# Kernel tuning notes

Hardware: AMD Instinct MI355X
Metric: run time of the kernel (lower is better)

Reference implementation:

```python
import jax, jax.numpy as jnp
import numpy as np

TOP_K = 2
EPS = 1e-9


def setup_inputs() -> dict:
    key = jax.random.key(0)
    k1, k2, k3, k4 = jax.random.split(key, 4)
    B, T, D, H, E = 4, 2048, 1024, 4096, 8
    x = jax.random.normal(k1, (B, T, D), dtype=jnp.float32)
    Wr = jax.random.normal(k2, (D, E), dtype=jnp.float32) * 0.02
    W1 = jax.random.normal(k3, (E, D, H), dtype=jnp.float32) * 0.02
    W2 = jax.random.normal(k4, (E, H, D), dtype=jnp.float32) * 0.02
    return {"x": x, "Wr": Wr, "W1": W1, "W2": W2}


def reference(x, Wr, W1, W2):
    # x: (B,T,D); Wr: (D,E); W1: (E,D,H); W2: (E,H,D)
    E = Wr.shape[1]
    logits = jnp.einsum('btd,de->bte', x, Wr)          # (B,T,E)
    probs = jax.nn.softmax(logits, axis=-1)
    top_p, top_i = jax.lax.top_k(probs, TOP_K)         # (B,T,K)
    gates = top_p / (jnp.sum(top_p, axis=-1, keepdims=True) + EPS)
    # combine weights per expert: (B,T,E), zero where expert not selected
    oh = jax.nn.one_hot(top_i, E, dtype=x.dtype)       # (B,T,K,E)
    comb = jnp.sum(oh * gates[..., None], axis=2)      # (B,T,E)
    out = jnp.zeros_like(x)
    for e in range(E):  # fixed small expert loop
        h = jax.nn.gelu(jnp.einsum('btd,dh->bth', x, W1[e]), approximate=False)
        y = jnp.einsum('bth,hd->btd', h, W2[e])
        out = out + comb[..., e:e + 1] * y
    # load-balancing loss (on detached stats, matching torch .detach())
    mask = (jnp.sum(oh, axis=2) > 0).astype(jnp.float32)  # (B,T,E)
    imp = jnp.sum(jax.lax.stop_gradient(probs), axis=(0, 1))
    load = jnp.sum(jax.lax.stop_gradient(mask), axis=(0, 1))
    imp = imp / (jnp.sum(imp) + EPS)
    load = load / (jnp.sum(load) + EPS)
    lb = jnp.sum(imp * load) * E
    return out, lb
```

## Files before the change

### kernel.cpp

```cpp
#include <hip/hip_runtime.h>
#include <hip/hip_bf16.h>
#include <math.h>

#define NTOK 8192
#define DDIM 1024
#define HDIM 4096
#define NEXP 8
#define HROWS (NTOK*2 + 256)
#define RBLK 512

typedef unsigned int u32;
typedef unsigned short u16;
typedef __bf16 bf16x8 __attribute__((ext_vector_type(8)));
typedef float f32x4 __attribute__((ext_vector_type(4)));
typedef u16 u16x8 __attribute__((ext_vector_type(8)));
typedef u16 u16x4 __attribute__((ext_vector_type(4)));

__device__ __forceinline__ u16 f2bf(float f){
  u32 u = __builtin_bit_cast(u32, f);
  u32 r = (u + 0x7FFFu + ((u >> 16) & 1u)) >> 16;
  return (u16)r;
}
__device__ __forceinline__ float bf2f(u16 b){
  u32 u = ((u32)b) << 16;
  return __builtin_bit_cast(float, u);
}
__device__ __forceinline__ void gl_lds16(const void* g, void* l){
  __builtin_amdgcn_global_load_lds(
      (const __attribute__((address_space(1))) u32*)g,
      (__attribute__((address_space(3))) u32*)l, 16, 0, 0);
}
__device__ __forceinline__ float gelu_t(float v){
  float u = v * (0.7978845608f + 0.0356774081f * v * v);
  float e = __expf(2.0f * u);
  float t = 1.0f - 2.0f / (e + 1.0f);
  return 0.5f * v * (1.0f + t);
}

__global__ __launch_bounds__(256) void transpose_cvt(const float* __restrict__ in,
                                                     u16* __restrict__ out,
                                                     int R, int C){
  int e = blockIdx.z;
  const float* pin = in + (long)e * R * C;
  u16* pout = out + (long)e * R * C;
  __shared__ u16 tile[64][65];
  int c0 = blockIdx.x * 64, r0 = blockIdx.y * 64;
  int tid = threadIdx.x;
#pragma unroll
  for (int j = 0; j < 4; j++){
    int idx = tid + 256 * j;
    int r = idx >> 4, c4 = (idx & 15) << 2;
    float4 v = *(const float4*)(pin + (long)(r0 + r) * C + c0 + c4);
    tile[r][c4]     = f2bf(v.x);
    tile[r][c4 + 1] = f2bf(v.y);
    tile[r][c4 + 2] = f2bf(v.z);
    tile[r][c4 + 3] = f2bf(v.w);
  }
  __syncthreads();
#pragma unroll
  for (int j = 0; j < 4; j++){
    int idx = tid + 256 * j;
    int orow = idx >> 4, c4 = (idx & 15) << 2;
    u16x4 o;
    o[0] = tile[c4][orow];     o[1] = tile[c4 + 1][orow];
    o[2] = tile[c4 + 2][orow]; o[3] = tile[c4 + 3][orow];
    *(u16x4*)(pout + (long)(c0 + orow) * R + r0 + c4) = o;
  }
}

__global__ __launch_bounds__(1024) void route_kernel(const float* __restrict__ x,
                                                     const float* __restrict__ Wr,
                                                     u16* __restrict__ xb,
                                                     int4* __restrict__ meta,
                                                     float2* __restrict__ gates,
                                                     int* __restrict__ selrk,
                                                     int* __restrict__ blockhist,
                                                     float* __restrict__ impPart){
  const int wid = threadIdx.x >> 6;
  const int lane = threadIdx.x & 63;
  const int t = blockIdx.x * 16 + wid;
  const float* xr = x + (long)t * DDIM;
  u16* xbr = xb + (long)t * DDIM;
  float acc[NEXP] = {};
  for (int d0 = lane * 4; d0 < DDIM; d0 += 256){
    float4 xv = *(const float4*)(xr + d0);
    u16x4 xo;
    xo[0] = f2bf(xv.x); xo[1] = f2bf(xv.y); xo[2] = f2bf(xv.z); xo[3] = f2bf(xv.w);
    *(u16x4*)(xbr + d0) = xo;
    const float* w = Wr + d0 * NEXP;
#pragma unroll
    for (int q = 0; q < 4; q++){
      float xq = ((const float*)&xv)[q];
      float4 w0 = *(const float4*)(w + q * NEXP);
      float4 w1 = *(const float4*)(w + q * NEXP + 4);
      acc[0] += xq * w0.x; acc[1] += xq * w0.y; acc[2] += xq * w0.z; acc[3] += xq * w0.w;
      acc[4] += xq * w1.x; acc[5] += xq * w1.y; acc[6] += xq * w1.z; acc[7] += xq * w1.w;
    }
  }
#pragma unroll
  for (int e = 0; e < NEXP; e++){
#pragma unroll
    for (int off = 32; off; off >>= 1) acc[e] += __shfl_xor(acc[e], off, 64);
  }
  __shared__ int sel_s[32];
  __shared__ float p_s[16][NEXP];
  if (lane == 0){
    float mx = acc[0];
#pragma unroll
    for (int e = 1; e < NEXP; e++) mx = fmaxf(mx, acc[e]);
    float p[NEXP]; float s = 0.f;
#pragma unroll
    for (int e = 0; e < NEXP; e++){ p[e] = expf(acc[e] - mx); s += p[e]; }
    float inv = 1.f / s;
#pragma unroll
    for (int e = 0; e < NEXP; e++){ p[e] *= inv; p_s[wid][e] = p[e]; }
    int i0 = 0; float v0 = p[0];
#pragma unroll
    for (int e = 1; e < NEXP; e++) if (p[e] > v0){ v0 = p[e]; i0 = e; }
    int i1 = -1; float v1 = -1.f;
#pragma unroll
    for (int e = 0; e < NEXP; e++) if (e != i0 && p[e] > v1){ v1 = p[e]; i1 = e; }
    float gs = v0 + v1 + 1e-9f;
    meta[t] = make_int4(i0, i1, 0, 0);
    gates[t] = make_float2(v0 / gs, v1 / gs);
    sel_s[wid * 2] = i0;
    sel_s[wid * 2 + 1] = i1;
  }
  __syncthreads();
  const int tid = threadIdx.x;
  if (tid < 32){
    int e = sel_s[tid];
    int r = 0;
    for (int m = 0; m < tid; m++) r += (sel_s[m] == e) ? 1 : 0;
    selrk[blockIdx.x * 32 + tid] = (r << 3) | e;
  }
  if (tid < NEXP){
    int hcount = 0;
#pragma unroll
    for (int m = 0; m < 32; m++) hcount += (sel_s[m] == tid) ? 1 : 0;
    blockhist[blockIdx.x * NEXP + tid] = hcount;
    float s = 0.f;
#pragma unroll
    for (int w = 0; w < 16; w++) s += p_s[w][tid];
    impPart[blockIdx.x * NEXP + tid] = s;
  }
}

__global__ __launch_bounds__(512) void scan_kernel(int* __restrict__ blockhist,
                                                   const float* __restrict__ impPart,
                                                   int* __restrict__ cnt,
                                                   int* __restrict__ offs,
                                                   float* __restrict__ imp){
  const int e = threadIdx.x >> 6;
  const int lane = threadIdx.x & 63;
  const int base = lane * 8;
  int v[8]; int s = 0;
#pragma unroll
  for (int i = 0; i < 8; i++){
    int tmp = blockhist[(base + i) * NEXP + e];
    v[i] = s; s += tmp;
  }
  int inc = s;
#pragma unroll
  for (int off = 1; off < 64; off <<= 1){
    int o = __shfl_up(inc, off, 64);
    if (lane >= off) inc += o;
  }
  int excl = inc - s;
#pragma unroll
  for (int i = 0; i < 8; i++) blockhist[(base + i) * NEXP + e] = v[i] + excl;
  int tot = __shfl(inc, 63, 64);
  float fs = 0.f;
#pragma unroll
  for (int i = 0; i < 8; i++) fs += impPart[(base + i) * NEXP + e];
#pragma unroll
  for (int off = 32; off; off >>= 1) fs += __shfl_xor(fs, off, 64);
  __shared__ int cnt_s[NEXP];
  if (lane == 0){ cnt_s[e] = tot; cnt[e] = tot; imp[e] = fs; }
  __syncthreads();
  if (threadIdx.x == 0){
    int o = 0;
    for (int q = 0; q < NEXP; q++){ offs[q] = o; o += cnt_s[q]; }
  }
}

__global__ __launch_bounds__(256) void fill_kernel(const int* __restrict__ selrk,
                                                   const int* __restrict__ blockhist,
                                                   int* __restrict__ elist,
                                                   int4* __restrict__ meta){
  int m = blockIdx.x * 256 + threadIdx.x;
  int t = m >> 1, c = m & 1, b = m >> 5;
  int pk = selrk[m];
  int e = pk & 7, r = pk >> 3;
  int gslot = blockhist[b * NEXP + e] + r;
  elist[e * NTOK + gslot] = t;
  ((int*)meta)[t * 4 + 2 + c] = gslot;
}

template<int KD, int ND, bool GATHER, bool GELU>
__global__ __launch_bounds__(256) void gemm128_kernel(const u16* __restrict__ Ag,
                                                      const u16* __restrict__ Bg,
                                                      u16* __restrict__ Cg,
                                                      const int* __restrict__ elist,
                                                      const int* __restrict__ cnt,
                                                      const int* __restrict__ offs){
  const int NDB = ND / 128;
  const int bid = blockIdx.x;
  const int e  = bid & 7;
  const int le = bid >> 3;
  const int db = le % NDB;
  const int tt = le / NDB;
  const int n_e = cnt[e];
  if (tt * 128 >= n_e) return;
  const int cb = db * 128;
  __shared__ __align__(16) u16 As[128 * 64];
  __shared__ __align__(16) u16 Bs[128 * 64];
  const int tid = threadIdx.x;
  const int csrc = (((tid & 7) ^ ((tid >> 3) & 7)) << 3);
  const int clin = (tid & 7) << 3;
  const int row0 = offs[e] + tt * 128;
  const long bbase = ((long)e * ND + cb) * KD;
  long agb[4], bgb[4]; int lrow[4];
#pragma unroll
  for (int q = 0; q < 4; q++){
    int row = q * 32 + (tid >> 3);
    int arow;
    if (GATHER){
      int slot = tt * 128 + row;
      if (slot >= n_e) slot = n_e - 1;
      arow = elist[e * NTOK + slot];
    } else {
      arow = row0 + row;
    }
    lrow[q] = row;
    agb[q] = (long)arow * KD + csrc;
    bgb[q] = bbase + (long)row * KD + csrc;
  }
  const int wid = tid >> 6, lane = tid & 63;
  const int wr = (wid >> 1) * 64, wc = (wid & 1) * 64;
  const int fr = lane & 15, fq = lane >> 4;
  const int sw0 = (fq ^ (fr & 7)) << 3;
  const int sw1 = ((4 + fq) ^ (fr & 7)) << 3;
  const u16* aP0 = &As[(wr + fr) * 64 + sw0];
  const u16* aP1 = &As[(wr + fr) * 64 + sw1];
  const u16* bP0 = &Bs[(wc + fr) * 64 + sw0];
  const u16* bP1 = &Bs[(wc + fr) * 64 + sw1];
  f32x4 acc[4][4] = {};
  for (int kb = 0; kb < KD; kb += 64){
    __syncthreads();
#pragma unroll
    for (int q = 0; q < 4; q++){
      gl_lds16(Ag + agb[q] + kb, &As[lrow[q] * 64 + clin]);
      gl_lds16(Bg + bgb[q] + kb, &Bs[lrow[q] * 64 + clin]);
    }
    __syncthreads();
    {
      bf16x8 af[4], bfr[4];
#pragma unroll
      for (int m = 0; m < 4; m++) af[m] = *(const bf16x8*)(aP0 + m * 1024);
#pragma unroll
      for (int n = 0; n < 4; n++) bfr[n] = *(const bf16x8*)(bP0 + n * 1024);
#pragma unroll
      for (int m = 0; m < 4; m++)
#pragma unroll
        for (int n = 0; n < 4; n++)
          acc[m][n] = __builtin_amdgcn_mfma_f32_16x16x32_bf16(af[m], bfr[n], acc[m][n], 0, 0, 0);
    }
    {
      bf16x8 af[4], bfr[4];
#pragma unroll
      for (int m = 0; m < 4; m++) af[m] = *(const bf16x8*)(aP1 + m * 1024);
#pragma unroll
      for (int n = 0; n < 4; n++) bfr[n] = *(const bf16x8*)(bP1 + n * 1024);
#pragma unroll
      for (int m = 0; m < 4; m++)
#pragma unroll
        for (int n = 0; n < 4; n++)
          acc[m][n] = __builtin_amdgcn_mfma_f32_16x16x32_bf16(af[m], bfr[n], acc[m][n], 0, 0, 0);
    }
  }
#pragma unroll
  for (int m = 0; m < 4; m++){
#pragma unroll
    for (int j = 0; j < 4; j++){
      int row = wr + m * 16 + fq * 4 + j;
      int slot = tt * 128 + row;
      if (slot >= n_e) continue;
      long base = (long)(row0 + row) * ND + cb + wc;
#pragma unroll
      for (int n = 0; n < 4; n++){
        float v = acc[m][n][j];
        if (GELU) v = gelu_t(v);
        Cg[base + n * 16 + fr] = f2bf(v);
      }
    }
  }
}

__global__ __launch_bounds__(256) void combine_kernel(const u16* __restrict__ ypair,
                                                      const int4* __restrict__ meta,
                                                      const float2* __restrict__ gates,
                                                      const int* __restrict__ offs,
                                                      float* __restrict__ out){
  int t = blockIdx.x;
  int c = threadIdx.x;
  int4 m = meta[t];
  float2 g = gates[t];
  long p0 = (long)(offs[m.x] + m.z) * DDIM + c * 4;
  long p1 = (long)(offs[m.y] + m.w) * DDIM + c * 4;
  u16x4 y0 = *(const u16x4*)&ypair[p0];
  u16x4 y1 = *(const u16x4*)&ypair[p1];
  float4 o;
  o.x = g.x * bf2f(y0[0]) + g.y * bf2f(y1[0]);
  o.y = g.x * bf2f(y0[1]) + g.y * bf2f(y1[1]);
  o.z = g.x * bf2f(y0[2]) + g.y * bf2f(y1[2]);
  o.w = g.x * bf2f(y0[3]) + g.y * bf2f(y1[3]);
  *(float4*)&out[(long)t * DDIM + c * 4] = o;
}

__global__ void lb_kernel(const float* __restrict__ imp, const int* __restrict__ cnt,
                          float* __restrict__ outp){
  if (threadIdx.x == 0 && blockIdx.x == 0){
    float si = 0.f, sl = 0.f;
    for (int e = 0; e < NEXP; e++){ si += imp[e]; sl += (float)cnt[e]; }
    float lb = 0.f;
    for (int e = 0; e < NEXP; e++)
      lb += (imp[e] / (si + 1e-9f)) * ((float)cnt[e] / (sl + 1e-9f));
    outp[0] = lb * (float)NEXP;
  }
}

extern "C" void kernel_launch(void* const* d_in, const int* in_sizes, int n_in,
                              void* d_out, int out_size, void* d_ws, size_t ws_size,
                              hipStream_t stream){
  const float* x  = (const float*)d_in[0];
  const float* Wr = (const float*)d_in[1];
  const float* W1 = (const float*)d_in[2];
  const float* W2 = (const float*)d_in[3];
  float* out = (float*)d_out;
  char* ws = (char*)d_ws;
  size_t off = 0;
  u16* xb = (u16*)(ws + off);   off += (size_t)NTOK * DDIM * 2;
  u16* wt = (u16*)(ws + off);   off += (size_t)NEXP * DDIM * HDIM * 2;
  u16* h  = (u16*)(ws + off);   off += (size_t)HROWS * HDIM * 2;
  u16* yp = (u16*)(ws + off);   off += (size_t)NTOK * 2 * DDIM * 2;
  int* elist    = (int*)(ws + off);    off += (size_t)NEXP * NTOK * 4;
  int4* meta    = (int4*)(ws + off);   off += (size_t)NTOK * 16;
  float2* gts   = (float2*)(ws + off); off += (size_t)NTOK * 8;
  int* selrk    = (int*)(ws + off);    off += (size_t)NTOK * 2 * 4;
  int* bhist    = (int*)(ws + off);    off += (size_t)RBLK * NEXP * 4;
  float* impP   = (float*)(ws + off);  off += (size_t)RBLK * NEXP * 4;
  int* cnt      = (int*)(ws + off);    off += 32;
  float* imp    = (float*)(ws + off);  off += 32;
  int* offs     = (int*)(ws + off);    off += 32;
  if (ws_size < off) return;

  route_kernel<<<RBLK, 1024, 0, stream>>>(x, Wr, xb, meta, gts, selrk, bhist, impP);
  scan_kernel<<<1, 512, 0, stream>>>(bhist, impP, cnt, offs, imp);
  fill_kernel<<<NTOK * 2 / 256, 256, 0, stream>>>(selrk, bhist, elist, meta);
  transpose_cvt<<<dim3(HDIM / 64, DDIM / 64, NEXP), 256, 0, stream>>>(W1, wt, DDIM, HDIM);
  gemm128_kernel<DDIM, HDIM, true, true><<<NEXP * (NTOK / 128) * (HDIM / 128), 256, 0, stream>>>(
      xb, wt, h, elist, cnt, offs);
  transpose_cvt<<<dim3(DDIM / 64, HDIM / 64, NEXP), 256, 0, stream>>>(W2, wt, HDIM, DDIM);
  gemm128_kernel<HDIM, DDIM, false, false><<<NEXP * (NTOK / 128) * (DDIM / 128), 256, 0, stream>>>(
      h, wt, yp, elist, cnt, offs);
  combine_kernel<<<NTOK, 256, 0, stream>>>(yp, meta, gts, offs, out);
  lb_kernel<<<1, 64, 0, stream>>>(imp, cnt, out + (size_t)NTOK * DDIM);
}
```

Before: 531.6 us.

## Rewrite expert GEMM with 128x256 tiles and triple-buffered async LDS pipeline

Replaces the 128x128, K=64 single-buffered GEMM with a 128x256 tile at K=32 and a three-stage LDS ring buffer. Global-to-LDS loads for step k+2 are issued while step k computes, using explicit vmcnt waits and one barrier per step, and LDS reads use inline ds_read_b128 with a new swizzle. The aim is to hide global load latency and raise MFMA work per loaded byte. The cost is more registers (32 accumulators per thread) and more LDS, along with launch_bounds requesting 2 blocks per CU.

```diff
diff --git a/kernel.cpp b/kernel.cpp
--- a/kernel.cpp
+++ b/kernel.cpp
@@ -13,6 +13,7 @@
 typedef unsigned short u16;
 typedef __bf16 bf16x8 __attribute__((ext_vector_type(8)));
 typedef float f32x4 __attribute__((ext_vector_type(4)));
+typedef u32 u32x4 __attribute__((ext_vector_type(4)));
 typedef u16 u16x8 __attribute__((ext_vector_type(8)));
 typedef u16 u16x4 __attribute__((ext_vector_type(4)));
 
@@ -198,13 +199,13 @@
 }
 
 template<int KD, int ND, bool GATHER, bool GELU>
-__global__ __launch_bounds__(256) void gemm128_kernel(const u16* __restrict__ Ag,
-                                                      const u16* __restrict__ Bg,
-                                                      u16* __restrict__ Cg,
-                                                      const int* __restrict__ elist,
-                                                      const int* __restrict__ cnt,
-                                                      const int* __restrict__ offs){
-  const int NDB = ND / 128;
+__global__ __launch_bounds__(256, 2) void gemm_tb(const u16* __restrict__ Ag,
+                                                  const u16* __restrict__ Bg,
+                                                  u16* __restrict__ Cg,
+                                                  const int* __restrict__ elist,
+                                                  const int* __restrict__ cnt,
+                                                  const int* __restrict__ offs){
+  const int NDB = ND / 256;
   const int bid = blockIdx.x;
   const int e  = bid & 7;
   const int le = bid >> 3;
@@ -212,18 +213,16 @@
   const int tt = le / NDB;
   const int n_e = cnt[e];
   if (tt * 128 >= n_e) return;
-  const int cb = db * 128;
-  __shared__ __align__(16) u16 As[128 * 64];
-  __shared__ __align__(16) u16 Bs[128 * 64];
+  const int cb = db * 256;
+  __shared__ __align__(16) u16 As[3][128 * 32];
+  __shared__ __align__(16) u16 Bs[3][256 * 32];
   const int tid = threadIdx.x;
-  const int csrc = (((tid & 7) ^ ((tid >> 3) & 7)) << 3);
-  const int clin = (tid & 7) << 3;
+  const int sch = (((tid & 3) ^ ((tid >> 2) & 3) ^ ((tid >> 4) & 3)) << 3);
   const int row0 = offs[e] + tt * 128;
-  const long bbase = ((long)e * ND + cb) * KD;
-  long agb[4], bgb[4]; int lrow[4];
-#pragma unroll
-  for (int q = 0; q < 4; q++){
-    int row = q * 32 + (tid >> 3);
+  long agb[2];
+#pragma unroll
+  for (int i = 0; i < 2; i++){
+    int row = i * 64 + (tid >> 2);
     int arow;
     if (GATHER){
       int slot = tt * 128 + row;
@@ -232,58 +231,84 @@
     } else {
       arow = row0 + row;
     }
-    lrow[q] = row;
-    agb[q] = (long)arow * KD + csrc;
-    bgb[q] = bbase + (long)row * KD + csrc;
-  }
-  const int wid = tid >> 6, lane = tid & 63;
-  const int wr = (wid >> 1) * 64, wc = (wid & 1) * 64;
+    agb[i] = (long)arow * KD + sch;
+  }
+  const long bbase = ((long)e * ND + cb) * KD;
+  long bgb[4];
+#pragma unroll
+  for (int j = 0; j < 4; j++)
+    bgb[j] = bbase + (long)(j * 64 + (tid >> 2)) * KD + sch;
+  const int ldst = tid * 8;
+
+  const int lane = tid & 63;
+  const int w = tid >> 6;
+  const int wc = w * 64;
   const int fr = lane & 15, fq = lane >> 4;
-  const int sw0 = (fq ^ (fr & 7)) << 3;
-  const int sw1 = ((4 + fq) ^ (fr & 7)) << 3;
-  const u16* aP0 = &As[(wr + fr) * 64 + sw0];
-  const u16* aP1 = &As[(wr + fr) * 64 + sw1];
-  const u16* bP0 = &Bs[(wc + fr) * 64 + sw0];
-  const u16* bP1 = &Bs[(wc + fr) * 64 + sw1];
-  f32x4 acc[4][4] = {};
-  for (int kb = 0; kb < KD; kb += 64){
-    __syncthreads();
-#pragma unroll
-    for (int q = 0; q < 4; q++){
-      gl_lds16(Ag + agb[q] + kb, &As[lrow[q] * 64 + clin]);
-      gl_lds16(Bg + bgb[q] + kb, &Bs[lrow[q] * 64 + clin]);
-    }
-    __syncthreads();
-    {
-      bf16x8 af[4], bfr[4];
-#pragma unroll
-      for (int m = 0; m < 4; m++) af[m] = *(const bf16x8*)(aP0 + m * 1024);
-#pragma unroll
-      for (int n = 0; n < 4; n++) bfr[n] = *(const bf16x8*)(bP0 + n * 1024);
-#pragma unroll
-      for (int m = 0; m < 4; m++)
-#pragma unroll
-        for (int n = 0; n < 4; n++)
-          acc[m][n] = __builtin_amdgcn_mfma_f32_16x16x32_bf16(af[m], bfr[n], acc[m][n], 0, 0, 0);
-    }
-    {
-      bf16x8 af[4], bfr[4];
-#pragma unroll
-      for (int m = 0; m < 4; m++) af[m] = *(const bf16x8*)(aP1 + m * 1024);
-#pragma unroll
-      for (int n = 0; n < 4; n++) bfr[n] = *(const bf16x8*)(bP1 + n * 1024);
-#pragma unroll
-      for (int m = 0; m < 4; m++)
-#pragma unroll
-        for (int n = 0; n < 4; n++)
-          acc[m][n] = __builtin_amdgcn_mfma_f32_16x16x32_bf16(af[m], bfr[n], acc[m][n], 0, 0, 0);
-    }
-  }
-#pragma unroll
-  for (int m = 0; m < 4; m++){
+  const int swz = ((fq ^ (fr & 3) ^ ((fr >> 2) & 3)) << 4);
+  const u32 aB0 = (u32)(uintptr_t)&As[0][0] + (u32)(fr * 64 + swz);
+  const u32 bB0 = (u32)(uintptr_t)&Bs[0][0] + (u32)((wc + fr) * 64 + swz);
+
+  f32x4 acc[8][4] = {};
+  const int NK = KD / 32;
+
+#define STG(cbuf, kel) \
+    gl_lds16(Ag + agb[0] + (kel), &As[cbuf][0 * 2048 + ldst]); \
+    gl_lds16(Ag + agb[1] + (kel), &As[cbuf][1 * 2048 + ldst]); \
+    gl_lds16(Bg + bgb[0] + (kel), &Bs[cbuf][0 * 2048 + ldst]); \
+    gl_lds16(Bg + bgb[1] + (kel), &Bs[cbuf][1 * 2048 + ldst]); \
+    gl_lds16(Bg + bgb[2] + (kel), &Bs[cbuf][2 * 2048 + ldst]); \
+    gl_lds16(Bg + bgb[3] + (kel), &Bs[cbuf][3 * 2048 + ldst]);
+
+  STG(0, 0)
+  STG(1, 32)
+  asm volatile("s_waitcnt vmcnt(6)" ::: "memory");
+  __builtin_amdgcn_s_barrier();
+
+  int c = 0;
+  for (int k = 0; k < NK; ++k){
+    if (k + 2 < NK){
+      int cn = c + 2; if (cn >= 3) cn -= 3;
+      STG(cn, (k + 2) * 32)
+    }
+    const u32 aA = aB0 + (u32)(c * 8192);
+    const u32 bA = bB0 + (u32)(c * 16384);
+    u32x4 a[8], b[4];
+    asm volatile("ds_read_b128 %0, %1"             : "=v"(a[0]) : "v"(aA));
+    asm volatile("ds_read_b128 %0, %1 offset:1024" : "=v"(a[1]) : "v"(aA));
+    asm volatile("ds_read_b128 %0, %1 offset:2048" : "=v"(a[2]) : "v"(aA));
+    asm volatile("ds_read_b128 %0, %1 offset:3072" : "=v"(a[3]) : "v"(aA));
+    asm volatile("ds_read_b128 %0, %1 offset:4096" : "=v"(a[4]) : "v"(aA));
+    asm volatile("ds_read_b128 %0, %1 offset:5120" : "=v"(a[5]) : "v"(aA));
+    asm volatile("ds_read_b128 %0, %1 offset:6144" : "=v"(a[6]) : "v"(aA));
+    asm volatile("ds_read_b128 %0, %1 offset:7168" : "=v"(a[7]) : "v"(aA));
+    asm volatile("ds_read_b128 %0, %1"             : "=v"(b[0]) : "v"(bA));
+    asm volatile("ds_read_b128 %0, %1 offset:1024" : "=v"(b[1]) : "v"(bA));
+    asm volatile("ds_read_b128 %0, %1 offset:2048" : "=v"(b[2]) : "v"(bA));
+    asm volatile("ds_read_b128 %0, %1 offset:3072" : "=v"(b[3]) : "v"(bA));
+    asm volatile("s_waitcnt lgkmcnt(0)" ::: "memory");
+    __builtin_amdgcn_sched_barrier(0);
+#pragma unroll
+    for (int m = 0; m < 8; m++)
+#pragma unroll
+      for (int n = 0; n < 4; n++)
+        acc[m][n] = __builtin_amdgcn_mfma_f32_16x16x32_bf16(
+            __builtin_bit_cast(bf16x8, a[m]), __builtin_bit_cast(bf16x8, b[n]),
+            acc[m][n], 0, 0, 0);
+    if (k + 2 < NK){
+      asm volatile("s_waitcnt vmcnt(6)" ::: "memory");
+    } else if (k + 1 < NK){
+      asm volatile("s_waitcnt vmcnt(0)" ::: "memory");
+    }
+    if (k + 1 < NK) __builtin_amdgcn_s_barrier();
+    c += 1; if (c >= 3) c -= 3;
+  }
+#undef STG
+
+#pragma unroll
+  for (int m = 0; m < 8; m++){
 #pragma unroll
     for (int j = 0; j < 4; j++){
-      int row = wr + m * 16 + fq * 4 + j;
+      int row = m * 16 + fq * 4 + j;
       int slot = tt * 128 + row;
       if (slot >= n_e) continue;
       long base = (long)(row0 + row) * ND + cb + wc;
@@ -359,10 +384,10 @@
   scan_kernel<<<1, 512, 0, stream>>>(bhist, impP, cnt, offs, imp);
   fill_kernel<<<NTOK * 2 / 256, 256, 0, stream>>>(selrk, bhist, elist, meta);
   transpose_cvt<<<dim3(HDIM / 64, DDIM / 64, NEXP), 256, 0, stream>>>(W1, wt, DDIM, HDIM);
-  gemm128_kernel<DDIM, HDIM, true, true><<<NEXP * (NTOK / 128) * (HDIM / 128), 256, 0, stream>>>(
+  gemm_tb<DDIM, HDIM, true, true><<<NEXP * (NTOK / 128) * (HDIM / 256), 256, 0, stream>>>(
       xb, wt, h, elist, cnt, offs);
   transpose_cvt<<<dim3(DDIM / 64, HDIM / 64, NEXP), 256, 0, stream>>>(W2, wt, HDIM, DDIM);
-  gemm128_kernel<HDIM, DDIM, false, false><<<NEXP * (NTOK / 128) * (DDIM / 128), 256, 0, stream>>>(
+  gemm_tb<HDIM, DDIM, false, false><<<NEXP * (NTOK / 128) * (DDIM / 256), 256, 0, stream>>>(
       h, wt, yp, elist, cnt, offs);
   combine_kernel<<<NTOK, 256, 0, stream>>>(yp, meta, gts, offs, out);
   lb_kernel<<<1, 64, 0, stream>>>(imp, cnt, out + (size_t)NTOK * DDIM);
```

New measurement: 502.9 us. 5.4% less time.
